# Performance work log

Measured on AMD Instinct MI355X. Metric: run time of the kernel, lower is better.

## Reference

```python
import jax, jax.numpy as jnp
import numpy as np

N_QUBITS = 10
LAYERS = 4


def _ry(theta):
    c = jnp.cos(theta / 2).astype(jnp.complex64)
    s = jnp.sin(theta / 2).astype(jnp.complex64)
    return jnp.array([[c, -s], [s, c]], dtype=jnp.complex64)


def _rot(phi, theta, omega):
    # Rot = RZ(omega) RY(theta) RZ(phi)  (PennyLane convention)
    c = jnp.cos(theta / 2)
    s = jnp.sin(theta / 2)
    e_mm = jnp.exp(-0.5j * (phi + omega))
    e_pm = jnp.exp(0.5j * (phi - omega))
    e_mp = jnp.exp(-0.5j * (phi - omega))
    e_pp = jnp.exp(0.5j * (phi + omega))
    return jnp.array([[e_mm * c, -e_pm * s], [e_mp * s, e_pp * c]], dtype=jnp.complex64)


def _apply_1q(state, U, q):
    # state: (2,)*n complex; contract qubit axis q with 2x2 gate
    s = jnp.tensordot(U, state, axes=[[1], [q]])
    return jnp.moveaxis(s, 0, q)


def _apply_cnot(state, c, t):
    s = jnp.moveaxis(state, (c, t), (0, 1))
    s = jnp.stack([s[0], s[1, ::-1]], axis=0)
    return jnp.moveaxis(s, (0, 1), (c, t))


def _circuit(angles, weights):
    # angles: (n_qubits,) float32, weights: (layers, n_qubits, 3) float32
    n = N_QUBITS
    state = jnp.zeros((2 ** n,), dtype=jnp.complex64).at[0].set(1.0).reshape((2,) * n)
    for q in range(n):  # RY angle embedding
        state = _apply_1q(state, _ry(angles[q]), q)
    for l in range(LAYERS):  # strongly-entangling layers
        for q in range(n):
            state = _apply_1q(state, _rot(weights[l, q, 0], weights[l, q, 1], weights[l, q, 2]), q)
        for q in range(n):  # CNOT ring
            state = _apply_cnot(state, q, (q + 1) % n)
    probs = state.real ** 2 + state.imag ** 2  # (2,)*n
    zexp = []
    for q in range(n):
        p = probs.sum(axis=tuple(a for a in range(n) if a != q))
        zexp.append(p[0] - p[1])
    return jnp.stack(zexp)  # (n_qubits,)


def setup_inputs() -> dict:
    key = jax.random.key(0)
    ks = jax.random.split(key, 6)
    B, D = 8192, 784
    return {
        "x": jax.random.normal(ks[0], (B, D), dtype=jnp.float32),
        "Wp": jax.random.normal(ks[1], (N_QUBITS, D), dtype=jnp.float32) * (1.0 / np.sqrt(D)),
        "bp": jax.random.normal(ks[2], (N_QUBITS,), dtype=jnp.float32) * 0.01,
        "q_weights": jax.random.normal(ks[3], (LAYERS, N_QUBITS, 3), dtype=jnp.float32) * 0.01,
        "Wo": jax.random.normal(ks[4], (10, N_QUBITS), dtype=jnp.float32) * (1.0 / np.sqrt(N_QUBITS)),
        "bo": jax.random.normal(ks[5], (10,), dtype=jnp.float32) * 0.01,
    }


def reference(x, Wp, bp, q_weights, Wo, bo):
    # input projection + tanh
    h = jnp.tanh(x @ Wp.T + bp)  # (B, n_qubits)
    # batched quantum circuit (vmapped statevector simulation)
    q_out = jax.vmap(_circuit, in_axes=(0, None))(h, q_weights)  # (B, n_qubits)
    return q_out @ Wo.T + bo  # (B, 10) logits
```

## Files before the change

### kernel.cpp

```cpp
#include <hip/hip_runtime.h>
#include <hip/hip_bf16.h>

#define NQ      10
#define NLAYERS 4
#define D_IN    784
#define BLOCK   64


typedef __attribute__((ext_vector_type(2))) float f2;

__device__ __forceinline__ f2 cswapneg(f2 v) {
    f2 r; r.x = -v.y; r.y = v.x; return r;
}

template<int LB>
__device__ __forceinline__ float lane_xor(float v) {
    if constexpr (LB == 1) {
        return __int_as_float(__builtin_amdgcn_update_dpp(
            0, __float_as_int(v), 0xB1, 0xF, 0xF, false));
    } else if constexpr (LB == 2) {
        return __int_as_float(__builtin_amdgcn_update_dpp(
            0, __float_as_int(v), 0x4E, 0xF, 0xF, false));
    } else {
        return __shfl_xor(v, LB, 64);
    }
}

template<int LB>
__device__ __forceinline__ f2 lane_xor2(f2 v) {
    f2 r; r.x = lane_xor<LB>(v.x); r.y = lane_xor<LB>(v.y); return r;
}

template<int P>
__device__ __forceinline__ void rot_gate2(f2 (&a)[16], f2 (&b)[16], int lane,
                                          float4 gA, float4 gB) {
    if constexpr (P >= 4) {
        const int lb = 1 << (P - 4);
        const bool hi = (lane & lb) != 0;
        const float gdx = hi ? gB.z : gA.x, gdy = hi ? gB.w : gA.y;
        const float gox = hi ? gB.x : gA.z, goy = hi ? gB.y : gA.w;
#pragma unroll
        for (int r = 0; r < 16; r++) {
            f2 oa = lane_xor2<lb>(a[r]);
            f2 ob = lane_xor2<lb>(b[r]);
            f2 va = a[r], vb = b[r];
            a[r] = gdx * va + gdy * cswapneg(va) + gox * oa + goy * cswapneg(oa);
            b[r] = gdx * vb + gdy * cswapneg(vb) + gox * ob + goy * cswapneg(ob);
        }
    } else {
        const int m = 1 << P;
#pragma unroll
        for (int r = 0; r < 16; r++) {
            if (!(r & m)) {
                const int r1 = r | m;
                f2 A0 = a[r], A1 = a[r1];
                f2 B0 = b[r], B1 = b[r1];
                f2 ia0 = cswapneg(A0), ia1 = cswapneg(A1);
                f2 ib0 = cswapneg(B0), ib1 = cswapneg(B1);
                a[r]  = gA.x * A0 + gA.y * ia0 + gA.z * A1 + gA.w * ia1;
                b[r]  = gA.x * B0 + gA.y * ib0 + gA.z * B1 + gA.w * ib1;
                a[r1] = gB.x * A0 + gB.y * ia0 + gB.z * A1 + gB.w * ia1;
                b[r1] = gB.x * B0 + gB.y * ib0 + gB.z * B1 + gB.w * ib1;
            }
        }
    }
}

template<int P>
__device__ __forceinline__ void rot_gate2ab(f2 (&a)[16], f2 (&b)[16], int lane,
                                            float4 aAm, float4 aBm,
                                            float4 bAm, float4 bBm) {
    if constexpr (P >= 4) {
        const int lb = 1 << (P - 4);
        const bool hi = (lane & lb) != 0;
        const float adx = hi ? aBm.z : aAm.x, ady = hi ? aBm.w : aAm.y;
        const float aox = hi ? aBm.x : aAm.z, aoy = hi ? aBm.y : aAm.w;
        const float bdx = hi ? bBm.z : bAm.x, bdy = hi ? bBm.w : bAm.y;
        const float box = hi ? bBm.x : bAm.z, boy = hi ? bBm.y : bAm.w;
#pragma unroll
        for (int r = 0; r < 16; r++) {
            f2 oa = lane_xor2<lb>(a[r]);
            f2 ob = lane_xor2<lb>(b[r]);
            f2 va = a[r], vb = b[r];
            a[r] = adx * va + ady * cswapneg(va) + aox * oa + aoy * cswapneg(oa);
            b[r] = bdx * vb + bdy * cswapneg(vb) + box * ob + boy * cswapneg(ob);
        }
    } else {
        const int m = 1 << P;
#pragma unroll
        for (int r = 0; r < 16; r++) {
            if (!(r & m)) {
                const int r1 = r | m;
                f2 A0 = a[r], A1 = a[r1];
                f2 B0 = b[r], B1 = b[r1];
                f2 ia0 = cswapneg(A0), ia1 = cswapneg(A1);
                f2 ib0 = cswapneg(B0), ib1 = cswapneg(B1);
                a[r]  = aAm.x * A0 + aAm.y * ia0 + aAm.z * A1 + aAm.w * ia1;
                b[r]  = bAm.x * B0 + bAm.y * ib0 + bAm.z * B1 + bAm.w * ib1;
                a[r1] = aBm.x * A0 + aBm.y * ia0 + aBm.z * A1 + aBm.w * ia1;
                b[r1] = bBm.x * B0 + bBm.y * ib0 + bBm.z * B1 + bBm.w * ib1;
            }
        }
    }
}

__device__ __forceinline__ void rot9_fused2(f2 (&a)[16], f2 (&b)[16], int lane,
                                            float4 gA, float4 gB) {
    const bool hi = (lane & 32) != 0;
    const float gdx = hi ? gB.z : gA.x, gdy = hi ? gB.w : gA.y;
    const float gox = hi ? gB.x : gA.z, goy = hi ? gB.y : gA.w;
#pragma unroll
    for (int r = 0; r < 16; r++) {
        f2 oa; oa.x = __shfl_xor(a[r].x, 32, 64); oa.y = __shfl_xor(a[r].y, 32, 64);
        f2 ob; ob.x = __shfl_xor(b[r].x, 32, 64); ob.y = __shfl_xor(b[r].y, 32, 64);
        f2 va = a[r], vb = b[r];
        if (!(r & 1)) {
            a[r] = gdx * va + gdy * cswapneg(va) + gox * oa + goy * cswapneg(oa);
            b[r] = gdx * vb + gdy * cswapneg(vb) + gox * ob + goy * cswapneg(ob);
        } else {
            a[r] = gdx * oa + gdy * cswapneg(oa) + gox * va + goy * cswapneg(va);
            b[r] = gdx * ob + gdy * cswapneg(ob) + gox * vb + goy * cswapneg(vb);
        }
    }
}

template<int PC, int PT>
__device__ __forceinline__ void cnot_gate2(f2 (&a)[16], f2 (&b)[16], int lane) {
    if constexpr (PC >= 4 && PT < 4) {
        const int mt = 1 << PT;
        const bool ctl = (lane & (1 << (PC - 4))) != 0;
#pragma unroll
        for (int r = 0; r < 16; r++) {
            if (!(r & mt)) {
                const int r1 = r | mt;
                f2 A0 = a[r], A1 = a[r1], B0 = b[r], B1 = b[r1];
                f2 na0, na1, nb0, nb1;
                na0.x = ctl ? A1.x : A0.x;  na0.y = ctl ? A1.y : A0.y;
                na1.x = ctl ? A0.x : A1.x;  na1.y = ctl ? A0.y : A1.y;
                nb0.x = ctl ? B1.x : B0.x;  nb0.y = ctl ? B1.y : B0.y;
                nb1.x = ctl ? B0.x : B1.x;  nb1.y = ctl ? B0.y : B1.y;
                a[r] = na0; a[r1] = na1; b[r] = nb0; b[r1] = nb1;
            }
        }
    } else if constexpr (PC < 4 && PT >= 4) {
        const int mc = 1 << PC, mt = 1 << (PT - 4);
#pragma unroll
        for (int r = 0; r < 16; r++) {
            if (r & mc) {
                a[r].x = __shfl_xor(a[r].x, mt, 64);
                a[r].y = __shfl_xor(a[r].y, mt, 64);
                b[r].x = __shfl_xor(b[r].x, mt, 64);
                b[r].y = __shfl_xor(b[r].y, mt, 64);
            }
        }
    } else {
        const int mc = 1 << PC, mt = 1 << PT;
#pragma unroll
        for (int r = 0; r < 16; r++) {
            if ((r & mc) && !(r & mt)) {
                const int r1 = r | mt;
                f2 t = a[r]; a[r] = a[r1]; a[r1] = t;
                f2 u = b[r]; b[r] = b[r1]; b[r1] = u;
            }
        }
    }
}

__global__ __launch_bounds__(BLOCK)
__attribute__((amdgpu_waves_per_eu(2, 8)))
void qnet_kernel(
    const float* __restrict__ x,
    const float* __restrict__ Wp,
    const float* __restrict__ bp,
    const float* __restrict__ qw,
    const float* __restrict__ Wo,
    const float* __restrict__ bo,
    float* __restrict__ out, int B)
{
    __shared__ __align__(16) float gates[NLAYERS * NQ * 8];

    const int lane = threadIdx.x;
    const int s0   = blockIdx.x * 2;
    const int s1   = s0 + 1;

    if (lane < NLAYERS * NQ) {
        float phi = qw[lane * 3 + 0];
        float th  = qw[lane * 3 + 1];
        float om  = qw[lane * 3 + 2];
        float s, c;   sincosf(0.5f * th, &s, &c);
        float sap, cap; sincosf(0.5f * (phi + om), &sap, &cap);
        float sam, cam; sincosf(0.5f * (phi - om), &sam, &cam);
        float* g = &gates[lane * 8];
        g[0] =  cap * c;  g[1] = -sap * c;
        g[2] = -cam * s;  g[3] = -sam * s;
        g[4] =  cam * s;  g[5] = -sam * s;
        g[6] =  cap * c;  g[7] =  sap * c;
    }
    __syncthreads();
    if (s0 >= B) return;

    float acc0[NQ], acc1[NQ];
#pragma unroll
    for (int q = 0; q < NQ; q++) { acc0[q] = 0.f; acc1[q] = 0.f; }
    const float* xr0 = x + (size_t)s0 * D_IN;
    const float* xr1 = x + (size_t)s1 * D_IN;
    for (int d = lane; d < D_IN; d += 64) {
        float x0 = xr0[d], x1 = xr1[d];
#pragma unroll
        for (int q = 0; q < NQ; q++) {
            float w = Wp[q * D_IN + d];
            acc0[q] += x0 * w;
            acc1[q] += x1 * w;
        }
    }
#pragma unroll
    for (int q = 0; q < NQ; q++) {
#pragma unroll
        for (int o = 1; o < 64; o <<= 1) {
            acc0[q] += __shfl_xor(acc0[q], o, 64);
            acc1[q] += __shfl_xor(acc1[q], o, 64);
        }
    }
    float myc0 = 1.f, mys0 = 0.f, myc1 = 1.f, mys1 = 0.f;
    if (lane < NQ) {
        float h0 = tanhf(acc0[lane] + bp[lane]);
        float h1 = tanhf(acc1[lane] + bp[lane]);
        sincosf(0.5f * h0, &mys0, &myc0);
        sincosf(0.5f * h1, &mys1, &myc1);
    }

    f2 a[16], b[16];
#pragma unroll
    for (int r = 0; r < 16; r++) { a[r].x = 0.f; a[r].y = 0.f; b[r].x = 0.f; b[r].y = 0.f; }
    if (lane == 0) { a[0].x = 1.f; b[0].x = 1.f; }

    const int bidx = (lane ^ (lane >> 1)) << 2;

    {
        const float* gl = &gates[0];
        float c0, ss0, c1, ss1;
#define FROTQ(Q) \
        c0 = __shfl(myc0, Q, 64); ss0 = __shfl(mys0, Q, 64); \
        c1 = __shfl(myc1, Q, 64); ss1 = __shfl(mys1, Q, 64); \
        { float4 gA = *(const float4*)(gl + Q * 8); \
          float4 gB = *(const float4*)(gl + Q * 8 + 4); \
          float4 aAm, aBm, bAm, bBm; \
          aAm.x = gA.x * c0 + gA.z * ss0;  aAm.y = gA.y * c0 + gA.w * ss0; \
          aAm.z = gA.z * c0 - gA.x * ss0;  aAm.w = gA.w * c0 - gA.y * ss0; \
          aBm.x = gB.x * c0 + gB.z * ss0;  aBm.y = gB.y * c0 + gB.w * ss0; \
          aBm.z = gB.z * c0 - gB.x * ss0;  aBm.w = gB.w * c0 - gB.y * ss0; \
          bAm.x = gA.x * c1 + gA.z * ss1;  bAm.y = gA.y * c1 + gA.w * ss1; \
          bAm.z = gA.z * c1 - gA.x * ss1;  bAm.w = gA.w * c1 - gA.y * ss1; \
          bBm.x = gB.x * c1 + gB.z * ss1;  bBm.y = gB.y * c1 + gB.w * ss1; \
          bBm.z = gB.z * c1 - gB.x * ss1;  bBm.w = gB.w * c1 - gB.y * ss1; \
          rot_gate2ab<9 - Q>(a, b, lane, aAm, aBm, bAm, bBm); }
        FROTQ(0) FROTQ(1) FROTQ(2) FROTQ(3) FROTQ(4)
        FROTQ(5) FROTQ(6) FROTQ(7) FROTQ(8) FROTQ(9)
#undef FROTQ
#pragma unroll
        for (int r = 0; r < 16; r++) {
            a[r].x = __int_as_float(__builtin_amdgcn_ds_bpermute(bidx, __float_as_int(a[r].x)));
            a[r].y = __int_as_float(__builtin_amdgcn_ds_bpermute(bidx, __float_as_int(a[r].y)));
            b[r].x = __int_as_float(__builtin_amdgcn_ds_bpermute(bidx, __float_as_int(b[r].x)));
            b[r].y = __int_as_float(__builtin_amdgcn_ds_bpermute(bidx, __float_as_int(b[r].y)));
        }
        cnot_gate2<4, 3>(a, b, lane);
        cnot_gate2<3, 2>(a, b, lane);
        cnot_gate2<2, 1>(a, b, lane);
        cnot_gate2<1, 0>(a, b, lane);
    }

    for (int l = 1; l < NLAYERS; l++) {
        const float* gl = &gates[l * NQ * 8];
        {   float4 gA = *(const float4*)(gl);
            float4 gB = *(const float4*)(gl + 4);
            rot9_fused2(a, b, lane, gA, gB); }
#define ROTQ(Q) { float4 gA = *(const float4*)(gl + Q * 8); \
                  float4 gB = *(const float4*)(gl + Q * 8 + 4); \
                  rot_gate2<9 - Q>(a, b, lane, gA, gB); }
        ROTQ(1) ROTQ(2) ROTQ(3) ROTQ(4)
        ROTQ(5) ROTQ(6) ROTQ(7) ROTQ(8) ROTQ(9)
#undef ROTQ
#pragma unroll
        for (int r = 0; r < 16; r++) {
            a[r].x = __int_as_float(__builtin_amdgcn_ds_bpermute(bidx, __float_as_int(a[r].x)));
            a[r].y = __int_as_float(__builtin_amdgcn_ds_bpermute(bidx, __float_as_int(a[r].y)));
            b[r].x = __int_as_float(__builtin_amdgcn_ds_bpermute(bidx, __float_as_int(b[r].x)));
            b[r].y = __int_as_float(__builtin_amdgcn_ds_bpermute(bidx, __float_as_int(b[r].y)));
        }
        cnot_gate2<4, 3>(a, b, lane);
        cnot_gate2<3, 2>(a, b, lane);
        cnot_gate2<2, 1>(a, b, lane);
        cnot_gate2<1, 0>(a, b, lane);
    }
    cnot_gate2<0, 9>(a, b, lane);

    float S0 = 0.f, za3 = 0.f, za2 = 0.f, za1 = 0.f, za0 = 0.f;
    float S1 = 0.f, zb3 = 0.f, zb2 = 0.f, zb1 = 0.f, zb0 = 0.f;
#pragma unroll
    for (int r = 0; r < 16; r++) {
        float pa = a[r].x * a[r].x + a[r].y * a[r].y;
        float pb = b[r].x * b[r].x + b[r].y * b[r].y;
        S0 += pa;  S1 += pb;
        za3 += (r & 8) ? -pa : pa;   zb3 += (r & 8) ? -pb : pb;
        za2 += (r & 4) ? -pa : pa;   zb2 += (r & 4) ? -pb : pb;
        za1 += (r & 2) ? -pa : pa;   zb1 += (r & 2) ? -pb : pb;
        za0 += (r & 1) ? -pa : pa;   zb0 += (r & 1) ? -pb : pb;
    }
    float zqa[NQ], zqb[NQ];
    zqa[6] = za3; zqa[7] = za2; zqa[8] = za1; zqa[9] = za0;
    zqb[6] = zb3; zqb[7] = zb2; zqb[8] = zb1; zqb[9] = zb0;
#pragma unroll
    for (int q = 0; q < 6; q++) {
        zqa[q] = ((lane >> (5 - q)) & 1) ? -S0 : S0;
        zqb[q] = ((lane >> (5 - q)) & 1) ? -S1 : S1;
    }
#pragma unroll
    for (int q = 0; q < NQ; q++) {
#pragma unroll
        for (int o = 1; o < 64; o <<= 1) {
            zqa[q] += __shfl_xor(zqa[q], o, 64);
            zqb[q] += __shfl_xor(zqb[q], o, 64);
        }
    }

    if (lane < NQ) {
        const float* wrow = Wo + lane * NQ;
        float o0 = bo[lane], o1 = o0;
#pragma unroll
        for (int q = 0; q < NQ; q++) {
            float w = wrow[q];
            o0 += zqa[q] * w;
            o1 += zqb[q] * w;
        }
        out[(size_t)s0 * NQ + lane] = o0;
        out[(size_t)s1 * NQ + lane] = o1;
    }
}

extern "C" void kernel_launch(void* const* d_in, const int* in_sizes, int n_in,
                              void* d_out, int out_size, void* d_ws, size_t ws_size,
                              hipStream_t stream) {
    const float* x  = (const float*)d_in[0];
    const float* Wp = (const float*)d_in[1];
    const float* bp = (const float*)d_in[2];
    const float* qw = (const float*)d_in[3];
    const float* Wo = (const float*)d_in[4];
    const float* bo = (const float*)d_in[5];
    float* out = (float*)d_out;

    const int B = in_sizes[0] / D_IN;
    const int blocks = (B + 1) / 2;
    hipLaunchKernelGGL(qnet_kernel, dim3(blocks), dim3(BLOCK), 0, stream,
                       x, Wp, bp, qw, Wo, bo, out, B);
}
```

Baseline: 167.1 us.

## Simulate one sample per wavefront with four waves per block

Each wavefront now simulates a single sample's statevector instead of two interleaved ones, and each 256-thread block holds four waves, so it covers four samples and shares one gate-table setup. Halving the per-thread state (16 complex values instead of 32) lowers register pressure, and waves_per_eu is raised to 8 to push occupancy. The cost is less instruction-level parallelism per wave and Wp loads that are no longer shared between two samples, so latency hiding depends more on having more waves resident.

```diff
diff --git a/kernel.cpp b/kernel.cpp
--- a/kernel.cpp
+++ b/kernel.cpp
@@ -1,10 +1,9 @@
 #include <hip/hip_runtime.h>
-#include <hip/hip_bf16.h>
 
 #define NQ      10
 #define NLAYERS 4
 #define D_IN    784
-#define BLOCK   64
+#define BLOCK   256
 
 
 typedef __attribute__((ext_vector_type(2))) float f2;
@@ -32,8 +31,7 @@
 }
 
 template<int P>
-__device__ __forceinline__ void rot_gate2(f2 (&a)[16], f2 (&b)[16], int lane,
-                                          float4 gA, float4 gB) {
+__device__ __forceinline__ void rot_gate(f2 (&a)[16], int lane, float4 gA, float4 gB) {
     if constexpr (P >= 4) {
         const int lb = 1 << (P - 4);
         const bool hi = (lane & lb) != 0;
@@ -42,10 +40,8 @@
 #pragma unroll
         for (int r = 0; r < 16; r++) {
             f2 oa = lane_xor2<lb>(a[r]);
-            f2 ob = lane_xor2<lb>(b[r]);
-            f2 va = a[r], vb = b[r];
+            f2 va = a[r];
             a[r] = gdx * va + gdy * cswapneg(va) + gox * oa + goy * cswapneg(oa);
-            b[r] = gdx * vb + gdy * cswapneg(vb) + gox * ob + goy * cswapneg(ob);
         }
     } else {
         const int m = 1 << P;
@@ -54,78 +50,32 @@
             if (!(r & m)) {
                 const int r1 = r | m;
                 f2 A0 = a[r], A1 = a[r1];
-                f2 B0 = b[r], B1 = b[r1];
                 f2 ia0 = cswapneg(A0), ia1 = cswapneg(A1);
-                f2 ib0 = cswapneg(B0), ib1 = cswapneg(B1);
                 a[r]  = gA.x * A0 + gA.y * ia0 + gA.z * A1 + gA.w * ia1;
-                b[r]  = gA.x * B0 + gA.y * ib0 + gA.z * B1 + gA.w * ib1;
                 a[r1] = gB.x * A0 + gB.y * ia0 + gB.z * A1 + gB.w * ia1;
-                b[r1] = gB.x * B0 + gB.y * ib0 + gB.z * B1 + gB.w * ib1;
-            }
-        }
-    }
-}
-
-template<int P>
-__device__ __forceinline__ void rot_gate2ab(f2 (&a)[16], f2 (&b)[16], int lane,
-                                            float4 aAm, float4 aBm,
-                                            float4 bAm, float4 bBm) {
-    if constexpr (P >= 4) {
-        const int lb = 1 << (P - 4);
-        const bool hi = (lane & lb) != 0;
-        const float adx = hi ? aBm.z : aAm.x, ady = hi ? aBm.w : aAm.y;
-        const float aox = hi ? aBm.x : aAm.z, aoy = hi ? aBm.y : aAm.w;
-        const float bdx = hi ? bBm.z : bAm.x, bdy = hi ? bBm.w : bAm.y;
-        const float box = hi ? bBm.x : bAm.z, boy = hi ? bBm.y : bAm.w;
-#pragma unroll
-        for (int r = 0; r < 16; r++) {
-            f2 oa = lane_xor2<lb>(a[r]);
-            f2 ob = lane_xor2<lb>(b[r]);
-            f2 va = a[r], vb = b[r];
-            a[r] = adx * va + ady * cswapneg(va) + aox * oa + aoy * cswapneg(oa);
-            b[r] = bdx * vb + bdy * cswapneg(vb) + box * ob + boy * cswapneg(ob);
-        }
-    } else {
-        const int m = 1 << P;
-#pragma unroll
-        for (int r = 0; r < 16; r++) {
-            if (!(r & m)) {
-                const int r1 = r | m;
-                f2 A0 = a[r], A1 = a[r1];
-                f2 B0 = b[r], B1 = b[r1];
-                f2 ia0 = cswapneg(A0), ia1 = cswapneg(A1);
-                f2 ib0 = cswapneg(B0), ib1 = cswapneg(B1);
-                a[r]  = aAm.x * A0 + aAm.y * ia0 + aAm.z * A1 + aAm.w * ia1;
-                b[r]  = bAm.x * B0 + bAm.y * ib0 + bAm.z * B1 + bAm.w * ib1;
-                a[r1] = aBm.x * A0 + aBm.y * ia0 + aBm.z * A1 + aBm.w * ia1;
-                b[r1] = bBm.x * B0 + bBm.y * ib0 + bBm.z * B1 + bBm.w * ib1;
-            }
-        }
-    }
-}
-
-__device__ __forceinline__ void rot9_fused2(f2 (&a)[16], f2 (&b)[16], int lane,
-                                            float4 gA, float4 gB) {
+            }
+        }
+    }
+}
+
+__device__ __forceinline__ void rot9_fused(f2 (&a)[16], int lane, float4 gA, float4 gB) {
     const bool hi = (lane & 32) != 0;
     const float gdx = hi ? gB.z : gA.x, gdy = hi ? gB.w : gA.y;
     const float gox = hi ? gB.x : gA.z, goy = hi ? gB.y : gA.w;
 #pragma unroll
     for (int r = 0; r < 16; r++) {
         f2 oa; oa.x = __shfl_xor(a[r].x, 32, 64); oa.y = __shfl_xor(a[r].y, 32, 64);
-        f2 ob; ob.x = __shfl_xor(b[r].x, 32, 64); ob.y = __shfl_xor(b[r].y, 32, 64);
-        f2 va = a[r], vb = b[r];
+        f2 va = a[r];
         if (!(r & 1)) {
             a[r] = gdx * va + gdy * cswapneg(va) + gox * oa + goy * cswapneg(oa);
-            b[r] = gdx * vb + gdy * cswapneg(vb) + gox * ob + goy * cswapneg(ob);
         } else {
             a[r] = gdx * oa + gdy * cswapneg(oa) + gox * va + goy * cswapneg(va);
-            b[r] = gdx * ob + gdy * cswapneg(ob) + gox * vb + goy * cswapneg(vb);
         }
     }
 }
 
 template<int PC, int PT>
-__device__ __forceinline__ void cnot_gate2(f2 (&a)[16], f2 (&b)[16], int lane) {
+__device__ __forceinline__ void cnot_gate(f2 (&a)[16], int lane) {
     if constexpr (PC >= 4 && PT < 4) {
         const int mt = 1 << PT;
         const bool ctl = (lane & (1 << (PC - 4))) != 0;
@@ -133,13 +83,11 @@
         for (int r = 0; r < 16; r++) {
             if (!(r & mt)) {
                 const int r1 = r | mt;
-                f2 A0 = a[r], A1 = a[r1], B0 = b[r], B1 = b[r1];
-                f2 na0, na1, nb0, nb1;
-                na0.x = ctl ? A1.x : A0.x;  na0.y = ctl ? A1.y : A0.y;
-                na1.x = ctl ? A0.x : A1.x;  na1.y = ctl ? A0.y : A1.y;
-                nb0.x = ctl ? B1.x : B0.x;  nb0.y = ctl ? B1.y : B0.y;
-                nb1.x = ctl ? B0.x : B1.x;  nb1.y = ctl ? B0.y : B1.y;
-                a[r] = na0; a[r1] = na1; b[r] = nb0; b[r1] = nb1;
+                f2 A0 = a[r], A1 = a[r1];
+                f2 n0, n1;
+                n0.x = ctl ? A1.x : A0.x;  n0.y = ctl ? A1.y : A0.y;
+                n1.x = ctl ? A0.x : A1.x;  n1.y = ctl ? A0.y : A1.y;
+                a[r] = n0; a[r1] = n1;
             }
         }
     } else if constexpr (PC < 4 && PT >= 4) {
@@ -149,8 +97,6 @@
             if (r & mc) {
                 a[r].x = __shfl_xor(a[r].x, mt, 64);
                 a[r].y = __shfl_xor(a[r].y, mt, 64);
-                b[r].x = __shfl_xor(b[r].x, mt, 64);
-                b[r].y = __shfl_xor(b[r].y, mt, 64);
             }
         }
     } else {
@@ -160,14 +106,13 @@
             if ((r & mc) && !(r & mt)) {
                 const int r1 = r | mt;
                 f2 t = a[r]; a[r] = a[r1]; a[r1] = t;
-                f2 u = b[r]; b[r] = b[r1]; b[r1] = u;
             }
         }
     }
 }
 
 __global__ __launch_bounds__(BLOCK)
-__attribute__((amdgpu_waves_per_eu(2, 8)))
+__attribute__((amdgpu_waves_per_eu(8, 8)))
 void qnet_kernel(
     const float* __restrict__ x,
     const float* __restrict__ Wp,
@@ -179,81 +124,66 @@
 {
     __shared__ __align__(16) float gates[NLAYERS * NQ * 8];
 
-    const int lane = threadIdx.x;
-    const int s0   = blockIdx.x * 2;
-    const int s1   = s0 + 1;
-
-    if (lane < NLAYERS * NQ) {
-        float phi = qw[lane * 3 + 0];
-        float th  = qw[lane * 3 + 1];
-        float om  = qw[lane * 3 + 2];
-        float s, c;   sincosf(0.5f * th, &s, &c);
+    const int tid  = threadIdx.x;
+    const int lane = tid & 63;
+    const int s    = blockIdx.x * (BLOCK / 64) + (tid >> 6);
+
+    if (tid < NLAYERS * NQ) {
+        float phi = qw[tid * 3 + 0];
+        float th  = qw[tid * 3 + 1];
+        float om  = qw[tid * 3 + 2];
+        float sth, cth; sincosf(0.5f * th, &sth, &cth);
         float sap, cap; sincosf(0.5f * (phi + om), &sap, &cap);
         float sam, cam; sincosf(0.5f * (phi - om), &sam, &cam);
-        float* g = &gates[lane * 8];
-        g[0] =  cap * c;  g[1] = -sap * c;
-        g[2] = -cam * s;  g[3] = -sam * s;
-        g[4] =  cam * s;  g[5] = -sam * s;
-        g[6] =  cap * c;  g[7] =  sap * c;
+        float* g = &gates[tid * 8];
+        g[0] =  cap * cth;  g[1] = -sap * cth;
+        g[2] = -cam * sth;  g[3] = -sam * sth;
+        g[4] =  cam * sth;  g[5] = -sam * sth;
+        g[6] =  cap * cth;  g[7] =  sap * cth;
     }
     __syncthreads();
-    if (s0 >= B) return;
-
-    float acc0[NQ], acc1[NQ];
-#pragma unroll
-    for (int q = 0; q < NQ; q++) { acc0[q] = 0.f; acc1[q] = 0.f; }
-    const float* xr0 = x + (size_t)s0 * D_IN;
-    const float* xr1 = x + (size_t)s1 * D_IN;
+    if (s >= B) return;
+
+    float acc[NQ];
+#pragma unroll
+    for (int q = 0; q < NQ; q++) acc[q] = 0.f;
+    const float* xr = x + (size_t)s * D_IN;
     for (int d = lane; d < D_IN; d += 64) {
-        float x0 = xr0[d], x1 = xr1[d];
-#pragma unroll
-        for (int q = 0; q < NQ; q++) {
-            float w = Wp[q * D_IN + d];
-            acc0[q] += x0 * w;
-            acc1[q] += x1 * w;
-        }
+        float xv = xr[d];
+#pragma unroll
+        for (int q = 0; q < NQ; q++) acc[q] += xv * Wp[q * D_IN + d];
     }
 #pragma unroll
     for (int q = 0; q < NQ; q++) {
 #pragma unroll
-        for (int o = 1; o < 64; o <<= 1) {
-            acc0[q] += __shfl_xor(acc0[q], o, 64);
-            acc1[q] += __shfl_xor(acc1[q], o, 64);
-        }
-    }
-    float myc0 = 1.f, mys0 = 0.f, myc1 = 1.f, mys1 = 0.f;
+        for (int o = 1; o < 64; o <<= 1) acc[q] += __shfl_xor(acc[q], o, 64);
+    }
+    float myc = 1.f, mys = 0.f;
     if (lane < NQ) {
-        float h0 = tanhf(acc0[lane] + bp[lane]);
-        float h1 = tanhf(acc1[lane] + bp[lane]);
-        sincosf(0.5f * h0, &mys0, &myc0);
-        sincosf(0.5f * h1, &mys1, &myc1);
-    }
-
-    f2 a[16], b[16];
-#pragma unroll
-    for (int r = 0; r < 16; r++) { a[r].x = 0.f; a[r].y = 0.f; b[r].x = 0.f; b[r].y = 0.f; }
-    if (lane == 0) { a[0].x = 1.f; b[0].x = 1.f; }
+        float h = tanhf(acc[lane] + bp[lane]);
+        sincosf(0.5f * h, &mys, &myc);
+    }
+
+    f2 a[16];
+#pragma unroll
+    for (int r = 0; r < 16; r++) { a[r].x = 0.f; a[r].y = 0.f; }
+    if (lane == 0) a[0].x = 1.f;
 
     const int bidx = (lane ^ (lane >> 1)) << 2;
 
     {
         const float* gl = &gates[0];
-        float c0, ss0, c1, ss1;
-#define FROTQ(Q) \
-        c0 = __shfl(myc0, Q, 64); ss0 = __shfl(mys0, Q, 64); \
-        c1 = __shfl(myc1, Q, 64); ss1 = __shfl(mys1, Q, 64); \
-        { float4 gA = *(const float4*)(gl + Q * 8); \
-          float4 gB = *(const float4*)(gl + Q * 8 + 4); \
-          float4 aAm, aBm, bAm, bBm; \
-          aAm.x = gA.x * c0 + gA.z * ss0;  aAm.y = gA.y * c0 + gA.w * ss0; \
-          aAm.z = gA.z * c0 - gA.x * ss0;  aAm.w = gA.w * c0 - gA.y * ss0; \
-          aBm.x = gB.x * c0 + gB.z * ss0;  aBm.y = gB.y * c0 + gB.w * ss0; \
-          aBm.z = gB.z * c0 - gB.x * ss0;  aBm.w = gB.w * c0 - gB.y * ss0; \
-          bAm.x = gA.x * c1 + gA.z * ss1;  bAm.y = gA.y * c1 + gA.w * ss1; \
-          bAm.z = gA.z * c1 - gA.x * ss1;  bAm.w = gA.w * c1 - gA.y * ss1; \
-          bBm.x = gB.x * c1 + gB.z * ss1;  bBm.y = gB.y * c1 + gB.w * ss1; \
-          bBm.z = gB.z * c1 - gB.x * ss1;  bBm.w = gB.w * c1 - gB.y * ss1; \
-          rot_gate2ab<9 - Q>(a, b, lane, aAm, aBm, bAm, bBm); }
+#define FROTQ(Q) { \
+        float c0  = __shfl(myc, Q, 64); \
+        float ss0 = __shfl(mys, Q, 64); \
+        float4 gA = *(const float4*)(gl + Q * 8); \
+        float4 gB = *(const float4*)(gl + Q * 8 + 4); \
+        float4 Am, Bm; \
+        Am.x = gA.x * c0 + gA.z * ss0;  Am.y = gA.y * c0 + gA.w * ss0; \
+        Am.z = gA.z * c0 - gA.x * ss0;  Am.w = gA.w * c0 - gA.y * ss0; \
+        Bm.x = gB.x * c0 + gB.z * ss0;  Bm.y = gB.y * c0 + gB.w * ss0; \
+        Bm.z = gB.z * c0 - gB.x * ss0;  Bm.w = gB.w * c0 - gB.y * ss0; \
+        rot_gate<9 - Q>(a, lane, Am, Bm); }
         FROTQ(0) FROTQ(1) FROTQ(2) FROTQ(3) FROTQ(4)
         FROTQ(5) FROTQ(6) FROTQ(7) FROTQ(8) FROTQ(9)
 #undef FROTQ
@@ -261,23 +191,21 @@
         for (int r = 0; r < 16; r++) {
             a[r].x = __int_as_float(__builtin_amdgcn_ds_bpermute(bidx, __float_as_int(a[r].x)));
             a[r].y = __int_as_float(__builtin_amdgcn_ds_bpermute(bidx, __float_as_int(a[r].y)));
-            b[r].x = __int_as_float(__builtin_amdgcn_ds_bpermute(bidx, __float_as_int(b[r].x)));
-            b[r].y = __int_as_float(__builtin_amdgcn_ds_bpermute(bidx, __float_as_int(b[r].y)));
-        }
-        cnot_gate2<4, 3>(a, b, lane);
-        cnot_gate2<3, 2>(a, b, lane);
-        cnot_gate2<2, 1>(a, b, lane);
-        cnot_gate2<1, 0>(a, b, lane);
+        }
+        cnot_gate<4, 3>(a, lane);
+        cnot_gate<3, 2>(a, lane);
+        cnot_gate<2, 1>(a, lane);
+        cnot_gate<1, 0>(a, lane);
     }
 
     for (int l = 1; l < NLAYERS; l++) {
         const float* gl = &gates[l * NQ * 8];
         {   float4 gA = *(const float4*)(gl);
             float4 gB = *(const float4*)(gl + 4);
-            rot9_fused2(a, b, lane, gA, gB); }
+            rot9_fused(a, lane, gA, gB); }
 #define ROTQ(Q) { float4 gA = *(const float4*)(gl + Q * 8); \
                   float4 gB = *(const float4*)(gl + Q * 8 + 4); \
-                  rot_gate2<9 - Q>(a, b, lane, gA, gB); }
+                  rot_gate<9 - Q>(a, lane, gA, gB); }
         ROTQ(1) ROTQ(2) ROTQ(3) ROTQ(4)
         ROTQ(5) ROTQ(6) ROTQ(7) ROTQ(8) ROTQ(9)
 #undef ROTQ
@@ -285,56 +213,44 @@
         for (int r = 0; r < 16; r++) {
             a[r].x = __int_as_float(__builtin_amdgcn_ds_bpermute(bidx, __float_as_int(a[r].x)));
             a[r].y = __int_as_float(__builtin_amdgcn_ds_bpermute(bidx, __float_as_int(a[r].y)));
-            b[r].x = __int_as_float(__builtin_amdgcn_ds_bpermute(bidx, __float_as_int(b[r].x)));
-            b[r].y = __int_as_float(__builtin_amdgcn_ds_bpermute(bidx, __float_as_int(b[r].y)));
-        }
-        cnot_gate2<4, 3>(a, b, lane);
-        cnot_gate2<3, 2>(a, b, lane);
-        cnot_gate2<2, 1>(a, b, lane);
-        cnot_gate2<1, 0>(a, b, lane);
-    }
-    cnot_gate2<0, 9>(a, b, lane);
-
-    float S0 = 0.f, za3 = 0.f, za2 = 0.f, za1 = 0.f, za0 = 0.f;
-    float S1 = 0.f, zb3 = 0.f, zb2 = 0.f, zb1 = 0.f, zb0 = 0.f;
+        }
+        cnot_gate<4, 3>(a, lane);
+        cnot_gate<3, 2>(a, lane);
+        cnot_gate<2, 1>(a, lane);
+        cnot_gate<1, 0>(a, lane);
+    }
+    cnot_gate<0, 9>(a, lane);
+
+    float S = 0.f, z3 = 0.f, z2 = 0.f, z1 = 0.f, z0 = 0.f;
 #pragma unroll
     for (int r = 0; r < 16; r++) {
         float pa = a[r].x * a[r].x + a[r].y * a[r].y;
-        float pb = b[r].x * b[r].x + b[r].y * b[r].y;
-        S0 += pa;  S1 += pb;
-        za3 += (r & 8) ? -pa : pa;   zb3 += (r & 8) ? -pb : pb;
-        za2 += (r & 4) ? -pa : pa;   zb2 += (r & 4) ? -pb : pb;
-        za1 += (r & 2) ? -pa : pa;   zb1 += (r & 2) ? -pb : pb;
-        za0 += (r & 1) ? -pa : pa;   zb0 += (r & 1) ? -pb : pb;
-    }
-    float zqa[NQ], zqb[NQ];
-    zqa[6] = za3; zqa[7] = za2; zqa[8] = za1; zqa[9] = za0;
-    zqb[6] = zb3; zqb[7] = zb2; zqb[8] = zb1; zqb[9] = zb0;
+        S += pa;
+        z3 += (r & 8) ? -pa : pa;
+        z2 += (r & 4) ? -pa : pa;
+        z1 += (r & 2) ? -pa : pa;
+        z0 += (r & 1) ? -pa : pa;
+    }
+    float zq[NQ];
+    zq[6] = z3; zq[7] = z2; zq[8] = z1; zq[9] = z0;
 #pragma unroll
     for (int q = 0; q < 6; q++) {
-        zqa[q] = ((lane >> (5 - q)) & 1) ? -S0 : S0;
-        zqb[q] = ((lane >> (5 - q)) & 1) ? -S1 : S1;
+        zq[q] = ((lane >> (5 - q)) & 1) ? -S : S;
     }
 #pragma unroll
     for (int q = 0; q < NQ; q++) {
 #pragma unroll
         for (int o = 1; o < 64; o <<= 1) {
-            zqa[q] += __shfl_xor(zqa[q], o, 64);
-            zqb[q] += __shfl_xor(zqb[q], o, 64);
+            zq[q] += __shfl_xor(zq[q], o, 64);
         }
     }
 
     if (lane < NQ) {
         const float* wrow = Wo + lane * NQ;
-        float o0 = bo[lane], o1 = o0;
-#pragma unroll
-        for (int q = 0; q < NQ; q++) {
-            float w = wrow[q];
-            o0 += zqa[q] * w;
-            o1 += zqb[q] * w;
-        }
-        out[(size_t)s0 * NQ + lane] = o0;
-        out[(size_t)s1 * NQ + lane] = o1;
+        float o0 = bo[lane];
+#pragma unroll
+        for (int q = 0; q < NQ; q++) o0 += zq[q] * wrow[q];
+        out[(size_t)s * NQ + lane] = o0;
     }
 }
 
@@ -350,7 +266,8 @@
     float* out = (float*)d_out;
 
     const int B = in_sizes[0] / D_IN;
-    const int blocks = (B + 1) / 2;
+    const int spb = BLOCK / 64;
+    const int blocks = (B + spb - 1) / spb;
     hipLaunchKernelGGL(qnet_kernel, dim3(blocks), dim3(BLOCK), 0, stream,
                        x, Wp, bp, qw, Wo, bo, out, B);
 }
```

Result: no change. 166.9 us (-0.1%).
